# Optimization experiments

Hardware: AMD Instinct MI355X
Metric: run time of the kernel (lower is better)

## Reference

```python
import jax, jax.numpy as jnp
import numpy as np

B, W, I, S, T, U, US = 4, 2000, 64, 64, 24, 32, 2
V, H, D, OUT = 32000, 4, 256, 512
PER = W + I + S + U + 1          # nodes per graph = 2161
N = B * PER                      # 8644 nodes
E_RAND = N * 16


def setup_inputs() -> dict:
    key = jax.random.key(0)
    ks = jax.random.split(key, 24)
    s = 0.02
    inp = {}
    inp["all_words"] = jax.random.randint(ks[0], (B * W,), 0, V)
    inp["image_feats"] = jax.random.normal(ks[1], (B * I, 2048), jnp.float32)
    inp["sentences"] = jax.random.randint(ks[2], (B, S, T), 0, V)
    inp["sentence_mask"] = jnp.ones((B, S, T), jnp.float32)
    inp["utterances"] = jax.random.randint(ks[3], (B, U, US), 0, S)
    inp["utterance_mask"] = jnp.ones((B, U, US), jnp.float32)
    inp["session_ids"] = (jnp.arange(B) + 1) * PER - 1   # last node of each graph
    src = jax.random.randint(ks[4], (E_RAND,), 0, N)
    dst = jax.random.randint(ks[5], (E_RAND,), 0, N)
    loop = jnp.arange(N)
    inp["edge_src"] = jnp.concatenate([src, loop])
    inp["edge_dst"] = jnp.concatenate([dst, loop])
    # learned parameters
    inp["word_embed"] = jax.random.normal(ks[6], (V, 300), jnp.float32) * s
    inp["text_fc_w"] = jax.random.normal(ks[7], (300, 1024), jnp.float32) * s
    inp["text_fc_b"] = jnp.zeros((1024,), jnp.float32)
    inp["image_fc_w"] = jax.random.normal(ks[8], (2048, 1024), jnp.float32) * s
    inp["image_fc_b"] = jnp.zeros((1024,), jnp.float32)
    inp["gat0_fc"] = jax.random.normal(ks[9], (1024, H * D), jnp.float32) * s
    inp["gat0_al"] = jax.random.normal(ks[10], (H, D), jnp.float32) * s
    inp["gat0_ar"] = jax.random.normal(ks[11], (H, D), jnp.float32) * s
    inp["gat0_b"] = jnp.zeros((H * D,), jnp.float32)
    inp["gat1_fc"] = jax.random.normal(ks[12], (H * D, H * D), jnp.float32) * s
    inp["gat1_al"] = jax.random.normal(ks[13], (H, D), jnp.float32) * s
    inp["gat1_ar"] = jax.random.normal(ks[14], (H, D), jnp.float32) * s
    inp["gat1_b"] = jnp.zeros((H * D,), jnp.float32)
    inp["gat2_fc"] = jax.random.normal(ks[15], (H * D, OUT), jnp.float32) * s
    inp["gat2_al"] = jax.random.normal(ks[16], (1, OUT), jnp.float32) * s
    inp["gat2_ar"] = jax.random.normal(ks[17], (1, OUT), jnp.float32) * s
    inp["gat2_b"] = jnp.zeros((OUT,), jnp.float32)
    return inp


def _gat_layer(h, src, dst, fc_w, al, ar, b, act):
    # DGL GATConv: fc -> per-head attention logits -> edge softmax over dst -> aggregate
    n = h.shape[0]
    nh, dd = al.shape
    f = (h @ fc_w).reshape(n, nh, dd)                    # [N,H,D]
    el = (f * al).sum(-1)                                # [N,H]
    er = (f * ar).sum(-1)
    e = jax.nn.leaky_relu(el[src] + er[dst], 0.2)        # [E,H]
    m = jax.ops.segment_max(e, dst, num_segments=n)      # stable softmax per dst node
    a = jnp.exp(e - m[dst])
    z = jax.ops.segment_sum(a, dst, num_segments=n)
    alpha = a / z[dst]                                   # [E,H]
    out = jax.ops.segment_sum(alpha[:, :, None] * f[src], dst, num_segments=n)
    out = out + b.reshape(nh, dd)
    if act:
        out = jax.nn.elu(out)
    return out.reshape(n, nh * dd)


def _masked_mean(x, mask):
    # x: [..., K, F], mask: [..., K]
    s = (x * mask[..., None]).sum(-2)
    cnt = mask.sum(-1, keepdims=True)
    cnt = jnp.where(cnt == 0, 1.0, cnt)
    return s / cnt


def reference(all_words, image_feats, sentences, sentence_mask, utterances,
              utterance_mask, session_ids, edge_src, edge_dst,
              word_embed, text_fc_w, text_fc_b, image_fc_w, image_fc_b,
              gat0_fc, gat0_al, gat0_ar, gat0_b,
              gat1_fc, gat1_al, gat1_ar, gat1_b,
              gat2_fc, gat2_al, gat2_ar, gat2_b):
    b, s_num, t_num = sentences.shape
    u_num, us_num = utterances.shape[1], utterances.shape[2]
    w_per = all_words.shape[0] // b
    i_per = image_feats.shape[0] // b

    # word nodes
    we = word_embed[all_words].reshape(b, w_per, 300)
    # sentence nodes: masked mean over words
    sw = word_embed[sentences]                           # [B,S,T,300]
    sent = _masked_mean(sw, sentence_mask)               # [B,S,300]
    # utterance nodes: gather sentence embeds, masked mean over sentences
    uidx = utterances.reshape(b, u_num * us_num)
    ue = jnp.take_along_axis(sent, uidx[:, :, None], axis=1).reshape(b, u_num, us_num, -1)
    utt = _masked_mean(ue, utterance_mask)               # [B,U,300]
    # session node
    sess = utt.mean(axis=1, keepdims=True)               # [B,1,300]

    txt = lambda x: x @ text_fc_w + text_fc_b
    wf, sf, uf, ssf = txt(we), txt(sent), txt(utt), txt(sess)
    imf = (image_feats @ image_fc_w + image_fc_b).reshape(b, i_per, -1)

    # node layout per graph: [words, images, sentences, utterances, session]
    h = jnp.concatenate([wf, imf, sf, uf, ssf], axis=1).reshape(-1, 1024)

    h = _gat_layer(h, edge_src, edge_dst, gat0_fc, gat0_al, gat0_ar, gat0_b, act=True)
    h = _gat_layer(h, edge_src, edge_dst, gat1_fc, gat1_al, gat1_ar, gat1_b, act=True)
    h = _gat_layer(h, edge_src, edge_dst, gat2_fc, gat2_al, gat2_ar, gat2_b, act=False)

    return h[session_ids]                                # [B, 512]
```

## Files before the change

kernel.cpp:

```cpp
#include <hip/hip_runtime.h>
#include <math.h>

constexpr int kB = 4, kW = 2000, kI = 64, kS = 64, kT = 24, kU = 32, kUS = 2;
constexpr int kPER = kW + kI + kS + kU + 1;
constexpr int kN   = kB * kPER;
constexpr int kTxtPer  = kW + kS + kU + 1;
constexpr int kTxtRows = kB * kTxtPer;
constexpr int kEmb = 300;
constexpr int kEmbPad = 320;
constexpr int kHid = 1024;
constexpr int kOut = 512;
constexpr int kCap = 256;
constexpr int kMaxDeg = 256;
constexpr int kNcB = 1152;
constexpr int kNB  = kN / 4;

typedef __attribute__((ext_vector_type(8))) short bf16x8;
typedef __attribute__((ext_vector_type(4))) float f32x4;
typedef __attribute__((ext_vector_type(2))) float f32x2;

__device__ __forceinline__ unsigned short f2bf(float f) {
  union { float f; unsigned int u; } x; x.f = f;
  unsigned int r = x.u + 0x7FFF + ((x.u >> 16) & 1);
  return (unsigned short)(r >> 16);
}
__device__ __forceinline__ float bf2f(unsigned short u) {
  union { unsigned int u; float f; } x; x.u = ((unsigned int)u) << 16;
  return x.f;
}
__device__ __forceinline__ float bflo(unsigned int u) {
  union { unsigned int u; float f; } x; x.u = u << 16; return x.f;
}
__device__ __forceinline__ float bfhi(unsigned int u) {
  union { unsigned int u; float f; } x; x.u = u & 0xFFFF0000u; return x.f;
}
__device__ __forceinline__ f32x2 bfpair(unsigned int u) {
  union { unsigned int ui[2]; f32x2 f; } x;
  x.ui[0] = u << 16;
  x.ui[1] = u & 0xFFFF0000u;
  return x.f;
}

__device__ __forceinline__ void gl16(const unsigned short* g, unsigned short* l) {
  __builtin_amdgcn_global_load_lds(
      (const __attribute__((address_space(1))) void*)g,
      (__attribute__((address_space(3))) void*)l,
      16, 0, 0);
}

__global__ __launch_bounds__(256) void k_prep0(
    const float* __restrict__ tx_w, unsigned short* __restrict__ o_tx,
    const float* __restrict__ im_w, unsigned short* __restrict__ o_im,
    const float* __restrict__ g0_w, unsigned short* __restrict__ o_g0,
    const float* __restrict__ g1_w, unsigned short* __restrict__ o_g1,
    const float* __restrict__ g2_w, unsigned short* __restrict__ o_g2,
    const float* __restrict__ img, unsigned short* __restrict__ o_img,
    const int* __restrict__ sents, const float* __restrict__ smask,
    const float* __restrict__ wemb, float* __restrict__ sent,
    int* __restrict__ rmt, int* __restrict__ rmi,
    int* __restrict__ cnt, float* __restrict__ Cimg, float* __restrict__ Cg2) {
  int b = blockIdx.x;
  int tid = threadIdx.x;
  int tx = tid & 31, ty = tid >> 5;

  const float* in = nullptr; unsigned short* out = nullptr; int K = 0, N = 0, Kpad = 0, nbx = 0;
  if (b < 320)                { in = tx_w; out = o_tx; K = kEmb; N = kHid; Kpad = kEmbPad; nbx = 32; }
  else if ((b -= 320) < 2048) { in = im_w; out = o_im; K = 2048; N = kHid; Kpad = 2048; nbx = 32; }
  else if ((b -= 2048) < 1024){ in = g0_w; out = o_g0; K = kHid; N = kHid; Kpad = kHid; nbx = 32; }
  else if ((b -= 1024) < 1024){ in = g1_w; out = o_g1; K = kHid; N = kHid; Kpad = kHid; nbx = 32; }
  else if ((b -= 1024) < 512) { in = g2_w; out = o_g2; K = kHid; N = kOut; Kpad = kHid; nbx = 16; }
  else if ((b -= 512) < 512) {
    int i = b * 1024 + tid * 4;
    float4 v = *(const float4*)(img + i);
    ushort4 o; o.x = f2bf(v.x); o.y = f2bf(v.y); o.z = f2bf(v.z); o.w = f2bf(v.w);
    *(ushort4*)(o_img + i) = o;
    return;
  } else if ((b -= 512) < 256) {
    __shared__ int idx[kT];
    __shared__ float mk[kT];
    __shared__ float s_cnt;
    if (tid < kT) { idx[tid] = sents[b * kT + tid]; mk[tid] = smask[b * kT + tid]; }
    __syncthreads();
    if (tid == 0) {
      float c = 0.f;
      for (int i = 0; i < kT; ++i) c += mk[i];
      s_cnt = (c == 0.f) ? 1.f : c;
    }
    __syncthreads();
    for (int d = tid; d < kEmb; d += 256) {
      float acc = 0.f;
      for (int i = 0; i < kT; ++i) acc += wemb[idx[i] * kEmb + d] * mk[i];
      sent[b * kEmb + d] = acc / s_cnt;
    }
    return;
  } else if ((b -= 256) < 34) {
    int i = b * 256 + tid;
    if (i < kTxtRows) {
      int g = i / kTxtPer, j = i - g * kTxtPer;
      int base = g * kPER;
      int node;
      if (j < kW)                 node = base + j;
      else if (j < kW + kS)       node = base + kW + kI + (j - kW);
      else if (j < kW + kS + kU)  node = base + kW + kI + kS + (j - kW - kS);
      else                        node = base + kW + kI + kS + kU;
      rmt[i] = node;
    }
    if (i < kB * kI) {
      int g = i >> 6;
      rmi[i] = g * kPER + kW + (i & 63);
    }
    return;
  } else if ((b -= 34) < 34) {
    int i = b * 256 + tid;
    if (i < kN) cnt[i] = 0;
    return;
  } else if ((b -= 34) < 256) {
    uint4 z = make_uint4(0u, 0u, 0u, 0u);
    ((uint4*)Cimg)[b * 256 + tid] = z;
    return;
  } else if ((b -= 256) < 128) {
    uint4 z = make_uint4(0u, 0u, 0u, 0u);
    ((uint4*)Cg2)[b * 256 + tid] = z;
    return;
  } else {
    b -= 128;
    int i = b * 256 + tid;
    uint4 z = make_uint4(0u, 0u, 0u, 0u);
    ((uint4*)(o_g0 + (size_t)1032 * kHid))[i] = z;
    ((uint4*)(o_g1 + (size_t)1032 * kHid))[i] = z;
    return;
  }

  int bx = b % nbx, by = b / nbx;
  __shared__ float t[32][33];
  int n = bx * 32 + tx;
#pragma unroll
  for (int j = 0; j < 4; ++j) {
    int k = by * 32 + ty + j * 8;
    t[ty + j * 8][tx] = (k < K) ? in[(size_t)k * N + n] : 0.f;
  }
  __syncthreads();
#pragma unroll
  for (int j = 0; j < 4; ++j) {
    int nn = bx * 32 + ty + j * 8;
    int kk = by * 32 + tx;
    out[(size_t)nn * Kpad + kk] = f2bf(t[tx][ty + j * 8]);
  }
}

__global__ __launch_bounds__(256) void k_utt_sess(const int* __restrict__ utts,
                                                  const float* __restrict__ umask,
                                                  const float* __restrict__ sent,
                                                  float* __restrict__ utt,
                                                  float* __restrict__ sess,
                                                  const float* __restrict__ g0_w,
                                                  const float* __restrict__ g1_w,
                                                  const float* __restrict__ g0_al,
                                                  const float* __restrict__ g0_ar,
                                                  const float* __restrict__ g1_al,
                                                  const float* __restrict__ g1_ar,
                                                  unsigned short* __restrict__ o_g0,
                                                  unsigned short* __restrict__ o_g1) {
  int blk = blockIdx.x;
  int tid = threadIdx.x;
  if (blk < kB * kU) {
    int bu = blk, b = bu / kU;
    __shared__ int idx[kUS];
    __shared__ float mk[kUS];
    __shared__ float s_cnt;
    if (tid < kUS) { idx[tid] = utts[bu * kUS + tid]; mk[tid] = umask[bu * kUS + tid]; }
    __syncthreads();
    if (tid == 0) {
      float c = 0.f;
      for (int i = 0; i < kUS; ++i) c += mk[i];
      s_cnt = (c == 0.f) ? 1.f : c;
    }
    __syncthreads();
    for (int d = tid; d < kEmb; d += 256) {
      float acc = 0.f;
      for (int i = 0; i < kUS; ++i) acc += sent[(b * kS + idx[i]) * kEmb + d] * mk[i];
      utt[bu * kEmb + d] = acc / s_cnt;
    }
  } else if (blk < kB * kU + kB) {
    int b = blk - kB * kU;
    for (int d = tid; d < kEmb; d += 256) {
      float acc = 0.f;
      for (int u = 0; u < kU; ++u) {
        float ua = 0.f, c = 0.f;
        for (int us = 0; us < kUS; ++us) {
          int i = (b * kU + u) * kUS + us;
          int sidx = utts[i];
          float m = umask[i];
          ua += sent[(b * kS + sidx) * kEmb + d] * m;
          c += m;
        }
        if (c == 0.f) c = 1.f;
        acc += ua / c;
      }
      sess[b * kEmb + d] = acc * (1.f / kU);
    }
  } else {
    int b = blk - (kB * kU + kB);
    int layer = b >> 7, rem = b & 127;
    int which = rem >> 6;
    int rem2 = rem & 63;
    int h = rem2 >> 4, kblk = rem2 & 15;
    const float* fc = layer ? g1_w : g0_w;
    const float* a  = layer ? (which ? g1_ar : g1_al) : (which ? g0_ar : g0_al);
    unsigned short* wt = layer ? o_g1 : o_g0;
    int kl = tid >> 2, q = tid & 3;
    int k = kblk * 64 + kl;
    float s = 0.f;
    const float* fr = fc + (size_t)k * kHid + h * 256 + q * 64;
    const float* av = a + h * 256 + q * 64;
    for (int d = 0; d < 64; ++d) s += fr[d] * av[d];
    s += __shfl_xor(s, 1);
    s += __shfl_xor(s, 2);
    if (q == 0) wt[(size_t)(1024 + which * 4 + h) * kHid + k] = f2bf(s);
  }
}

__global__ __launch_bounds__(256) void k_txtcount(const int* __restrict__ aw,
                                                  const float* __restrict__ wemb,
                                                  const float* __restrict__ sent,
                                                  const float* __restrict__ utt,
                                                  const float* __restrict__ sess,
                                                  unsigned short* __restrict__ txt,
                                                  const int* __restrict__ dst,
                                                  int* __restrict__ cnt, int E) {
  int blk = blockIdx.x;
  int tid = threadIdx.x;
  if (blk < kTxtRows) {
    int r = blk;
    int g = r / kTxtPer, j = r - g * kTxtPer;
    const float* src;
    if (j < kW)                 src = wemb + (size_t)aw[g * kW + j] * kEmb;
    else if (j < kW + kS)       src = sent + (size_t)(g * kS + (j - kW)) * kEmb;
    else if (j < kW + kS + kU)  src = utt  + (size_t)(g * kU + (j - kW - kS)) * kEmb;
    else                        src = sess + (size_t)g * kEmb;
    for (int d = tid; d < kEmbPad; d += 256)
      txt[(size_t)r * kEmbPad + d] = (d < kEmb) ? f2bf(src[d]) : (unsigned short)0;
  } else {
    int e = (blk - kTxtRows) * 256 + tid;
    if (e < E) atomicAdd(&cnt[dst[e]], 1);
  }
}

template <bool OBF, bool ELR>
__global__ __launch_bounds__(512) void k_mm2(const unsigned short* __restrict__ A,
                                             const unsigned short* __restrict__ Bt,
                                             const float* __restrict__ bias,
                                             const int* __restrict__ rmap,
                                             void* __restrict__ Cout,
                                             float* __restrict__ el,
                                             float* __restrict__ er,
                                             int M, int K, int NcB, int NcOut) {
  __shared__ __align__(16) unsigned short As[128 * 64];
  __shared__ __align__(16) unsigned short Bs[128 * 64];
  int nCol = NcB >> 7;
  int bi = blockIdx.x;
  int xcd = bi & 7, bj = bi >> 3;
  int colTile = bj % nCol;
  int rowTile = ((bj / nCol) << 3) + xcd;
  int row0 = rowTile << 7;
  if (row0 >= M) return;
  int col0 = colTile << 7;

  int tid = threadIdx.x;
  int wid = tid >> 6, lane = tid & 63, quad = lane >> 4, l16 = lane & 15;
  int wm = wid >> 1, wn = wid & 1;

  f32x4 acc[2][4];
  f32x4 zero4 = {0.f, 0.f, 0.f, 0.f};
#pragma unroll
  for (int i = 0; i < 2; ++i)
#pragma unroll
    for (int j = 0; j < 4; ++j) acc[i][j] = zero4;

  int lr = lane >> 3;
  int swc = (lane & 7) ^ lr;

  for (int k0 = 0; k0 < K; k0 += 64) {
    __syncthreads();
#pragma unroll
    for (int i = 0; i < 2; ++i) {
      int rb = i * 64 + wid * 8;
      int r = rb + lr;
      int grow = row0 + r;
      if (grow >= M) grow = row0;
      gl16(A + (size_t)grow * K + k0 + (swc << 3), &As[rb * 64]);
      int nrow = col0 + r;
      gl16(Bt + (size_t)nrow * K + k0 + (swc << 3), &Bs[rb * 64]);
    }
    __syncthreads();
#pragma unroll
    for (int s = 0; s < 2; ++s) {
      int cc = s * 4 + quad;
      bf16x8 aF[2], bF[4];
#pragma unroll
      for (int mi = 0; mi < 2; ++mi) {
        int r = wm * 32 + mi * 16 + l16;
        aF[mi] = *(const bf16x8*)&As[r * 64 + ((cc ^ (r & 7)) << 3)];
      }
#pragma unroll
      for (int ni = 0; ni < 4; ++ni) {
        int r = wn * 64 + ni * 16 + l16;
        bF[ni] = *(const bf16x8*)&Bs[r * 64 + ((cc ^ (r & 7)) << 3)];
      }
#pragma unroll
      for (int mi = 0; mi < 2; ++mi)
#pragma unroll
        for (int ni = 0; ni < 4; ++ni)
          acc[mi][ni] = __builtin_amdgcn_mfma_f32_16x16x32_bf16(aF[mi], bF[ni], acc[mi][ni], 0, 0, 0);
    }
  }

#pragma unroll
  for (int mi = 0; mi < 2; ++mi) {
#pragma unroll
    for (int ni = 0; ni < 4; ++ni) {
      int gm0 = row0 + wm * 32 + mi * 16 + quad * 4;
      int gn  = col0 + wn * 64 + ni * 16 + l16;
      float bv = (bias && gn < NcOut) ? bias[gn] : 0.f;
#pragma unroll
      for (int i = 0; i < 4; ++i) {
        int r = gm0 + i;
        if (r >= M) continue;
        float v = acc[mi][ni][i] + bv;
        if (gn < NcOut) {
          if (OBF) {
            int orow = rmap ? rmap[r] : r;
            ((unsigned short*)Cout)[(size_t)orow * NcOut + gn] = f2bf(v);
          } else {
            ((float*)Cout)[(size_t)r * NcOut + gn] = v;
          }
        } else if (ELR) {
          int gn2 = gn - NcOut;
          if (gn2 < 4)      el[r * 4 + gn2] = v;
          else if (gn2 < 8) er[r * 4 + gn2 - 4] = v;
        }
      }
    }
  }
}

__global__ __launch_bounds__(256) void k_mm_sk(const unsigned short* __restrict__ A,
                                               const unsigned short* __restrict__ Bt,
                                               const int* __restrict__ rowlist,
                                               float* __restrict__ C,
                                               int M, int K, int Nc, int Kc) {
  __shared__ __align__(16) unsigned short As[64 * 64];
  __shared__ __align__(16) unsigned short Bs[64 * 64];
  int tid = threadIdx.x;
  int wid = tid >> 6, lane = tid & 63, quad = lane >> 4, l16 = lane & 15;
  int row0 = blockIdx.y * 64, col0 = blockIdx.x * 64;
  int k0 = blockIdx.z * Kc;
  int k1 = k0 + Kc; if (k1 > K) k1 = K;

  f32x4 acc[4];
  f32x4 zero4 = {0.f, 0.f, 0.f, 0.f};
#pragma unroll
  for (int i = 0; i < 4; ++i) acc[i] = zero4;

  int lr = lane >> 3;
  int swc = (lane & 7) ^ lr;

  int arow[2];
#pragma unroll
  for (int i = 0; i < 2; ++i) {
    int grow = row0 + i * 32 + wid * 8 + lr;
    int ar = 0;
    if (grow < M) ar = rowlist ? rowlist[grow] : grow;
    arow[i] = ar;
  }

  for (int kk = k0; kk < k1; kk += 64) {
    __syncthreads();
#pragma unroll
    for (int i = 0; i < 2; ++i) {
      int rb = i * 32 + wid * 8;
      gl16(A + (size_t)arow[i] * K + kk + (swc << 3), &As[rb * 64]);
      int nrow = col0 + rb + lr;
      gl16(Bt + (size_t)nrow * K + kk + (swc << 3), &Bs[rb * 64]);
    }
    __syncthreads();
#pragma unroll
    for (int s = 0; s < 2; ++s) {
      int cc = s * 4 + quad;
      bf16x8 bF;
      {
        int r = wid * 16 + l16;
        bF = *(const bf16x8*)&Bs[r * 64 + ((cc ^ (r & 7)) << 3)];
      }
#pragma unroll
      for (int mi = 0; mi < 4; ++mi) {
        int r = mi * 16 + l16;
        bf16x8 aF = *(const bf16x8*)&As[r * 64 + ((cc ^ (r & 7)) << 3)];
        acc[mi] = __builtin_amdgcn_mfma_f32_16x16x32_bf16(aF, bF, acc[mi], 0, 0, 0);
      }
    }
  }
#pragma unroll
  for (int mi = 0; mi < 4; ++mi) {
#pragma unroll
    for (int i = 0; i < 4; ++i) {
      int r = row0 + mi * 16 + quad * 4 + i;
      int c = col0 + wid * 16 + l16;
      if (r < M) atomicAdd(&C[(size_t)r * Nc + c], acc[mi][i]);
    }
  }
}

__global__ void k_sk_epi(const float* __restrict__ Cw, const float* __restrict__ bias,
                         const int* __restrict__ rmap, unsigned short* __restrict__ out,
                         int M, int Nc) {
  int i = blockIdx.x * blockDim.x + threadIdx.x;
  if (i >= M * Nc) return;
  int r = i / Nc, c = i - r * Nc;
  out[(size_t)rmap[r] * Nc + c] = f2bf(Cw[i] + bias[c]);
}

__global__ void k_scan(int* __restrict__ deg, int* __restrict__ offs, int n) {
  __shared__ int part[1024];
  int tid = threadIdx.x;
  int per = (n + 1023) >> 10;
  int start = tid * per;
  int local = 0;
  for (int i = 0; i < per; ++i) { int idx = start + i; if (idx < n) local += deg[idx]; }
  part[tid] = local;
  __syncthreads();
  for (int off = 1; off < 1024; off <<= 1) {
    int add = (tid >= off) ? part[tid - off] : 0;
    __syncthreads();
    part[tid] += add;
    __syncthreads();
  }
  int run = (tid == 0) ? 0 : part[tid - 1];
  for (int i = 0; i < per; ++i) {
    int idx = start + i;
    if (idx < n) { offs[idx] = run; run += deg[idx]; }
  }
  if (tid == 1023) offs[n] = part[1023];
  __syncthreads();
  for (int i = tid; i < n; i += 1024) deg[i] = 0;
}

__global__ void k_fill(const int* __restrict__ src, const int* __restrict__ dst,
                       const int* __restrict__ offs, int* __restrict__ cur,
                       int* __restrict__ csr, int E) {
  int e = blockIdx.x * blockDim.x + threadIdx.x;
  if (e < E) {
    int d = dst[e];
    int slot = offs[d] + atomicAdd(&cur[d], 1);
    csr[slot] = src[e];
  }
}

__global__ __launch_bounds__(256) void k_agg3h(const unsigned short* __restrict__ f,
                                               const float* __restrict__ el,
                                               const float* __restrict__ er,
                                               const int* __restrict__ offs,
                                               const int* __restrict__ csr,
                                               const float* __restrict__ bias,
                                               unsigned short* __restrict__ out) {
  __shared__ uint2 ws[4][kMaxDeg];
  int bid = blockIdx.x;
  int xcd = bid & 7;
  int g = xcd & 3;
  int hh = xcd >> 2;
  int nb = bid >> 3;
  if (nb >= kNB) return;
  int tid = threadIdx.x;
  int wid = tid >> 6, lane = tid & 63;
  int v = nb * 4 + wid;

  int e0 = offs[v];
  int deg = offs[v + 1] - e0;
  if (deg > kMaxDeg) deg = kMaxDeg;

  float erv = er[v * 4 + g];

  if (deg <= 64) {
    int s = 0;
    float x = -1e30f;
    if (lane < deg) {
      s = csr[e0 + lane];
      x = el[s * 4 + g] + erv;
      x = x > 0.f ? x : 0.2f * x;
    }
    float m = x;
#pragma unroll
    for (int o = 32; o; o >>= 1) m = fmaxf(m, __shfl_xor(m, o));
    float w = expf(x - m);
    float zs = w;
#pragma unroll
    for (int o = 32; o; o >>= 1) zs += __shfl_xor(zs, o);
    w *= 1.f / zs;
    ws[wid][lane] = make_uint2(__float_as_uint(w), (unsigned)s);
  } else {
    float m = -1e30f;
    for (int base = 0; base < deg; base += 64) {
      int idx = base + lane;
      float x = -1e30f;
      if (idx < deg) {
        int s = csr[e0 + idx];
        x = el[s * 4 + g] + erv;
        x = x > 0.f ? x : 0.2f * x;
        ws[wid][idx] = make_uint2(__float_as_uint(x), (unsigned)s);
      }
      float mm = x;
#pragma unroll
      for (int o = 32; o; o >>= 1) mm = fmaxf(mm, __shfl_xor(mm, o));
      m = fmaxf(m, mm);
    }
    float zs = 0.f;
    for (int base = 0; base < deg; base += 64) {
      int idx = base + lane;
      if (idx < deg) {
        float w = expf(__uint_as_float(ws[wid][idx].x) - m);
        ws[wid][idx].x = __float_as_uint(w);
        zs += w;
      }
    }
#pragma unroll
    for (int o = 32; o; o >>= 1) zs += __shfl_xor(zs, o);
    float rz = 1.f / zs;
    for (int base = 0; base < deg; base += 64) {
      int idx = base + lane;
      if (idx < deg)
        ws[wid][idx].x = __float_as_uint(__uint_as_float(ws[wid][idx].x) * rz);
    }
  }

  int slot = lane >> 4, l16 = lane & 15;
  const char* fb = (const char*)f + (size_t)(g * 256 + hh * 128 + l16 * 8) * 2;
  f32x2 a01 = {0.f, 0.f}, a23 = {0.f, 0.f}, a45 = {0.f, 0.f}, a67 = {0.f, 0.f};
  f32x2 c01 = {0.f, 0.f}, c23 = {0.f, 0.f}, c45 = {0.f, 0.f}, c67 = {0.f, 0.f};
  int e = 0;
  for (; e + 8 <= deg; e += 8) {
    int i0 = e + slot, i1 = e + 4 + slot;
    uint2 t0 = ws[wid][i0]; uint2 t1 = ws[wid][i1];
    uint4 f0 = *(const uint4*)(fb + ((size_t)t0.y << 11));
    uint4 f1 = *(const uint4*)(fb + ((size_t)t1.y << 11));
    float w0 = __uint_as_float(t0.x), w1 = __uint_as_float(t1.x);
    f32x2 wv0 = {w0, w0}, wv1 = {w1, w1};
    a01 += wv0 * bfpair(f0.x); a23 += wv0 * bfpair(f0.y);
    a45 += wv0 * bfpair(f0.z); a67 += wv0 * bfpair(f0.w);
    c01 += wv1 * bfpair(f1.x); c23 += wv1 * bfpair(f1.y);
    c45 += wv1 * bfpair(f1.z); c67 += wv1 * bfpair(f1.w);
  }
  for (; e < deg; e += 4) {
    int idx = e + slot;
    if (idx < deg) {
      uint2 t = ws[wid][idx];
      uint4 fv = *(const uint4*)(fb + ((size_t)t.y << 11));
      float w = __uint_as_float(t.x);
      f32x2 wv = {w, w};
      a01 += wv * bfpair(fv.x); a23 += wv * bfpair(fv.y);
      a45 += wv * bfpair(fv.z); a67 += wv * bfpair(fv.w);
    }
  }
  a01 += c01; a23 += c23; a45 += c45; a67 += c67;
  float a0 = a01.x, a1 = a01.y, a2 = a23.x, a3 = a23.y;
  float a4 = a45.x, a5 = a45.y, a6 = a67.x, a7 = a67.y;
#pragma unroll
  for (int o = 16; o <= 32; o <<= 1) {
    a0 += __shfl_xor(a0, o); a1 += __shfl_xor(a1, o);
    a2 += __shfl_xor(a2, o); a3 += __shfl_xor(a3, o);
    a4 += __shfl_xor(a4, o); a5 += __shfl_xor(a5, o);
    a6 += __shfl_xor(a6, o); a7 += __shfl_xor(a7, o);
  }

  if (slot == 0) {
    int d0 = g * 256 + hh * 128 + l16 * 8;
    float4 b0 = *(const float4*)(bias + d0);
    float4 b1 = *(const float4*)(bias + d0 + 4);
    float o0 = a0 + b0.x, o1 = a1 + b0.y, o2 = a2 + b0.z, o3 = a3 + b0.w;
    float o4 = a4 + b1.x, o5 = a5 + b1.y, o6 = a6 + b1.z, o7 = a7 + b1.w;
    o0 = o0 > 0.f ? o0 : expm1f(o0);
    o1 = o1 > 0.f ? o1 : expm1f(o1);
    o2 = o2 > 0.f ? o2 : expm1f(o2);
    o3 = o3 > 0.f ? o3 : expm1f(o3);
    o4 = o4 > 0.f ? o4 : expm1f(o4);
    o5 = o5 > 0.f ? o5 : expm1f(o5);
    o6 = o6 > 0.f ? o6 : expm1f(o6);
    o7 = o7 > 0.f ? o7 : expm1f(o7);
    uint4 ov;
    ov.x = (unsigned)f2bf(o0) | ((unsigned)f2bf(o1) << 16);
    ov.y = (unsigned)f2bf(o2) | ((unsigned)f2bf(o3) << 16);
    ov.z = (unsigned)f2bf(o4) | ((unsigned)f2bf(o5) << 16);
    ov.w = (unsigned)f2bf(o6) | ((unsigned)f2bf(o7) << 16);
    *(uint4*)(out + (size_t)v * 1024 + d0) = ov;
  }
}

__global__ void k_rows2(const int* __restrict__ sid, const int* __restrict__ offs,
                        const int* __restrict__ csr, int* __restrict__ rowlist,
                        int* __restrict__ info) {
  __shared__ int degs[kB], starts[kB], total;
  int tid = threadIdx.x;
  int bv = tid >> 6, lane = tid & 63;
  if (tid < kB) {
    int v = sid[tid];
    degs[tid] = offs[v + 1] - offs[v];
  }
  __syncthreads();
  if (tid == 0) {
    int p = 0;
    for (int b = 0; b < kB; ++b) {
      starts[b] = p;
      int d = degs[b];
      if (p + d > kCap) d = kCap - p;
      degs[b] = d;
      p += d;
    }
    total = p;
  }
  __syncthreads();
  int v = sid[bv];
  int e0 = offs[v];
  int deg = degs[bv];
  int start = starts[bv];
  if (lane == 0) {
    info[bv] = start;
    info[4 + bv] = deg;
    info[8 + bv] = start;
  }
  __syncthreads();
  for (int idx = lane; idx < deg; idx += 64) {
    int s = csr[e0 + idx];
    rowlist[start + idx] = s;
    if (s == v) info[8 + bv] = start + idx;
  }
  for (int i = total + tid; i < kCap; i += 256) rowlist[i] = 0;
}

__global__ __launch_bounds__(256) void k_gat2fin(const float* __restrict__ fc,
                                                 const float* __restrict__ al,
                                                 const float* __restrict__ ar,
                                                 const int* __restrict__ info,
                                                 const float* __restrict__ bias,
                                                 float* __restrict__ out) {
  __shared__ float el_s[kCap], er_s[kCap];
  int bv = blockIdx.x;
  int tid = threadIdx.x;
  int wid = tid >> 6, lane = tid & 63;
  int start = info[bv], cnt = info[4 + bv];
  int selfI = info[8 + bv] - start;

  for (int i = wid; i < cnt; i += 4) {
    const float* row = fc + (size_t)(start + i) * 512 + lane * 8;
    float4 x0 = *(const float4*)(row);
    float4 x1 = *(const float4*)(row + 4);
    float4 a0 = *(const float4*)(al + lane * 8);
    float4 a1 = *(const float4*)(al + lane * 8 + 4);
    float4 r0 = *(const float4*)(ar + lane * 8);
    float4 r1 = *(const float4*)(ar + lane * 8 + 4);
    float a = x0.x * a0.x + x0.y * a0.y + x0.z * a0.z + x0.w * a0.w
            + x1.x * a1.x + x1.y * a1.y + x1.z * a1.z + x1.w * a1.w;
    float b = x0.x * r0.x + x0.y * r0.y + x0.z * r0.z + x0.w * r0.w
            + x1.x * r1.x + x1.y * r1.y + x1.z * r1.z + x1.w * r1.w;
#pragma unroll
    for (int o = 32; o; o >>= 1) {
      a += __shfl_xor(a, o);
      b += __shfl_xor(b, o);
    }
    if (lane == 0) { el_s[i] = a; er_s[i] = b; }
  }
  __syncthreads();

  float erv = er_s[selfI];
  float m = -1e30f;
  for (int i = 0; i < cnt; ++i) {
    float x = el_s[i] + erv;
    x = x > 0.f ? x : 0.2f * x;
    m = fmaxf(m, x);
  }
  float z = 0.f, s0 = 0.f, s1 = 0.f;
  for (int i = 0; i < cnt; ++i) {
    float x = el_s[i] + erv;
    x = x > 0.f ? x : 0.2f * x;
    float w = expf(x - m);
    z += w;
    s0 += w * fc[(size_t)(start + i) * 512 + tid];
    s1 += w * fc[(size_t)(start + i) * 512 + 256 + tid];
  }
  out[bv * 512 + tid] = s0 / z + bias[tid];
  out[bv * 512 + 256 + tid] = s1 / z + bias[256 + tid];
}

extern "C" void kernel_launch(void* const* d_in, const int* in_sizes, int n_in,
                              void* d_out, int out_size, void* d_ws, size_t ws_size,
                              hipStream_t stream) {
  const int*   all_words   = (const int*)d_in[0];
  const float* image_feats = (const float*)d_in[1];
  const int*   sentences   = (const int*)d_in[2];
  const float* sent_mask   = (const float*)d_in[3];
  const int*   utterances  = (const int*)d_in[4];
  const float* utt_mask    = (const float*)d_in[5];
  const int*   session_ids = (const int*)d_in[6];
  const int*   edge_src    = (const int*)d_in[7];
  const int*   edge_dst    = (const int*)d_in[8];
  const float* word_embed  = (const float*)d_in[9];
  const float* text_fc_w   = (const float*)d_in[10];
  const float* text_fc_b   = (const float*)d_in[11];
  const float* image_fc_w  = (const float*)d_in[12];
  const float* image_fc_b  = (const float*)d_in[13];
  const float* gat0_fc     = (const float*)d_in[14];
  const float* gat0_al     = (const float*)d_in[15];
  const float* gat0_ar     = (const float*)d_in[16];
  const float* gat0_b      = (const float*)d_in[17];
  const float* gat1_fc     = (const float*)d_in[18];
  const float* gat1_al     = (const float*)d_in[19];
  const float* gat1_ar     = (const float*)d_in[20];
  const float* gat1_b      = (const float*)d_in[21];
  const float* gat2_fc     = (const float*)d_in[22];
  const float* gat2_al     = (const float*)d_in[23];
  const float* gat2_ar     = (const float*)d_in[24];
  const float* gat2_b      = (const float*)d_in[25];

  const int E = in_sizes[7];

  char* base = (char*)d_ws;
  size_t off = 0;
  auto alloc = [&](size_t elems, size_t esz) -> void* {
    void* p = base + off;
    off += ((elems * esz + 255) / 256) * 256;
    return p;
  };
  unsigned short* Abf   = (unsigned short*)alloc((size_t)kN * kHid, 2);
  unsigned short* fbf   = (unsigned short*)alloc((size_t)kN * kHid, 2);
  unsigned short* txtbf = (unsigned short*)alloc((size_t)kTxtRows * kEmbPad, 2);
  unsigned short* imgbf = (unsigned short*)alloc((size_t)kB * kI * 2048, 2);
  unsigned short* wtTx  = (unsigned short*)alloc((size_t)kHid * kEmbPad, 2);
  unsigned short* wtIm  = (unsigned short*)alloc((size_t)kHid * 2048, 2);
  unsigned short* wtG0  = (unsigned short*)alloc((size_t)kNcB * kHid, 2);
  unsigned short* wtG1  = (unsigned short*)alloc((size_t)kNcB * kHid, 2);
  unsigned short* wtG2  = (unsigned short*)alloc((size_t)kOut * kHid, 2);
  float* Cimg   = (float*)alloc((size_t)kB * kI * kHid, 4);
  float* Cg2    = (float*)alloc((size_t)kCap * kOut, 4);
  float* sentb  = (float*)alloc((size_t)kB * kS * kEmb, 4);
  float* uttb   = (float*)alloc((size_t)kB * kU * kEmb, 4);
  float* sessb  = (float*)alloc((size_t)kB * kEmb, 4);
  float* el     = (float*)alloc((size_t)kN * 4, 4);
  float* er     = (float*)alloc((size_t)kN * 4, 4);
  int*   offs   = (int*)alloc(kN + 1, 4);
  int*   cnt    = (int*)alloc(kN, 4);
  int*   csr    = (int*)alloc(E, 4);
  int*   rmt    = (int*)alloc(kTxtRows, 4);
  int*   rmi    = (int*)alloc(kB * kI, 4);
  int*   rowl   = (int*)alloc(kCap, 4);
  int*   info   = (int*)alloc(16, 4);
  (void)ws_size; (void)n_in; (void)out_size;

  constexpr int kPrepBlocks = 320 + 2048 + 1024 + 1024 + 512 + 512 + 256 + 34 + 34 + 256 + 128 + 60;
  k_prep0<<<kPrepBlocks, 256, 0, stream>>>(
      text_fc_w, wtTx, image_fc_w, wtIm, gat0_fc, wtG0, gat1_fc, wtG1, gat2_fc, wtG2,
      image_feats, imgbf, sentences, sent_mask, word_embed, sentb, rmt, rmi,
      cnt, Cimg, Cg2);

  k_utt_sess<<<kB * kU + kB + 256, 256, 0, stream>>>(
      utterances, utt_mask, sentb, uttb, sessb,
      gat0_fc, gat1_fc, gat0_al, gat0_ar, gat1_al, gat1_ar, wtG0, wtG1);

  k_txtcount<<<kTxtRows + (E + 255) / 256, 256, 0, stream>>>(
      all_words, word_embed, sentb, uttb, sessb, txtbf, edge_dst, cnt, E);

  k_scan<<<1, 1024, 0, stream>>>(cnt, offs, kN);
  k_fill<<<(E + 255) / 256, 256, 0, stream>>>(edge_src, edge_dst, offs, cnt, csr, E);

  auto mmGrid = [](int M, int NcB_) {
    int nrt = (M + 127) / 128;
    return 8 * (NcB_ / 128) * ((nrt + 7) / 8);
  };

  k_mm2<true, false><<<mmGrid(kTxtRows, kHid), 512, 0, stream>>>(
      txtbf, wtTx, text_fc_b, rmt, Abf, nullptr, nullptr, kTxtRows, kEmbPad, kHid, kHid);

  k_mm_sk<<<dim3(kHid / 64, kB * kI / 64, 4), 256, 0, stream>>>(
      imgbf, wtIm, nullptr, Cimg, kB * kI, 2048, kHid, 512);
  k_sk_epi<<<(kB * kI * kHid + 255) / 256, 256, 0, stream>>>(
      Cimg, image_fc_b, rmi, Abf, kB * kI, kHid);

  k_mm2<true, true><<<mmGrid(kN, kNcB), 512, 0, stream>>>(
      Abf, wtG0, nullptr, nullptr, fbf, el, er, kN, kHid, kNcB, kHid);
  k_agg3h<<<8 * kNB, 256, 0, stream>>>(fbf, el, er, offs, csr, gat0_b, Abf);

  k_mm2<true, true><<<mmGrid(kN, kNcB), 512, 0, stream>>>(
      Abf, wtG1, nullptr, nullptr, fbf, el, er, kN, kHid, kNcB, kHid);
  k_agg3h<<<8 * kNB, 256, 0, stream>>>(fbf, el, er, offs, csr, gat1_b, Abf);

  k_rows2<<<1, 256, 0, stream>>>(session_ids, offs, csr, rowl, info);
  k_mm_sk<<<dim3(kOut / 64, kCap / 64, 4), 256, 0, stream>>>(
      Abf, wtG2, rowl, Cg2, kCap, kHid, kOut, 256);
  k_gat2fin<<<kB, 256, 0, stream>>>(Cg2, gat2_al, gat2_ar, info, gat2_b, (float*)d_out);
}
```

Before: 409.1 us.

## Split GAT aggregation into edge-softmax weight kernel and per-head gather kernel

Replaces the fused softmax-plus-aggregation kernel with two kernels. The first computes the edge softmax weights for all four heads at once and writes them to a global per-head weight array. The second gathers neighbour features, with each lane covering four channels of a full 256-wide head, and streams indices and weights straight from global memory. This removes the per-block redundant softmax work across the 8 head/half blocks and the LDS staging, at the cost of an extra launch and a global weight buffer round trip. It also drops the degree cap of 256.

```diff
diff --git a/kernel.cpp b/kernel.cpp
--- a/kernel.cpp
+++ b/kernel.cpp
@@ -11,9 +11,9 @@
 constexpr int kHid = 1024;
 constexpr int kOut = 512;
 constexpr int kCap = 256;
-constexpr int kMaxDeg = 256;
 constexpr int kNcB = 1152;
 constexpr int kNB  = kN / 4;
+constexpr int kNBhi = (kNB + 1) / 2;
 
 typedef __attribute__((ext_vector_type(8))) short bf16x8;
 typedef __attribute__((ext_vector_type(4))) float f32x4;
@@ -27,12 +27,6 @@
 __device__ __forceinline__ float bf2f(unsigned short u) {
   union { unsigned int u; float f; } x; x.u = ((unsigned int)u) << 16;
   return x.f;
-}
-__device__ __forceinline__ float bflo(unsigned int u) {
-  union { unsigned int u; float f; } x; x.u = u << 16; return x.f;
-}
-__device__ __forceinline__ float bfhi(unsigned int u) {
-  union { unsigned int u; float f; } x; x.u = u & 0xFFFF0000u; return x.f;
 }
 __device__ __forceinline__ f32x2 bfpair(unsigned int u) {
   union { unsigned int ui[2]; f32x2 f; } x;
@@ -456,142 +450,173 @@
   }
 }
 
-__global__ __launch_bounds__(256) void k_agg3h(const unsigned short* __restrict__ f,
-                                               const float* __restrict__ el,
+__global__ __launch_bounds__(256) void k_smaxw(const float* __restrict__ el,
                                                const float* __restrict__ er,
                                                const int* __restrict__ offs,
                                                const int* __restrict__ csr,
-                                               const float* __restrict__ bias,
-                                               unsigned short* __restrict__ out) {
-  __shared__ uint2 ws[4][kMaxDeg];
-  int bid = blockIdx.x;
-  int xcd = bid & 7;
-  int g = xcd & 3;
-  int hh = xcd >> 2;
-  int nb = bid >> 3;
-  if (nb >= kNB) return;
+                                               float* __restrict__ wcsr, int E) {
   int tid = threadIdx.x;
   int wid = tid >> 6, lane = tid & 63;
-  int v = nb * 4 + wid;
-
+  int v = blockIdx.x * 4 + wid;
   int e0 = offs[v];
   int deg = offs[v + 1] - e0;
-  if (deg > kMaxDeg) deg = kMaxDeg;
-
-  float erv = er[v * 4 + g];
+  float4 erv = *(const float4*)(er + (size_t)v * 4);
 
   if (deg <= 64) {
-    int s = 0;
-    float x = -1e30f;
+    float x0 = -1e30f, x1 = -1e30f, x2 = -1e30f, x3 = -1e30f;
     if (lane < deg) {
-      s = csr[e0 + lane];
-      x = el[s * 4 + g] + erv;
-      x = x > 0.f ? x : 0.2f * x;
-    }
-    float m = x;
-#pragma unroll
-    for (int o = 32; o; o >>= 1) m = fmaxf(m, __shfl_xor(m, o));
-    float w = expf(x - m);
-    float zs = w;
-#pragma unroll
-    for (int o = 32; o; o >>= 1) zs += __shfl_xor(zs, o);
-    w *= 1.f / zs;
-    ws[wid][lane] = make_uint2(__float_as_uint(w), (unsigned)s);
+      int s = csr[e0 + lane];
+      float4 e4 = *(const float4*)(el + (size_t)s * 4);
+      x0 = e4.x + erv.x; x1 = e4.y + erv.y; x2 = e4.z + erv.z; x3 = e4.w + erv.w;
+      x0 = x0 > 0.f ? x0 : 0.2f * x0;
+      x1 = x1 > 0.f ? x1 : 0.2f * x1;
+      x2 = x2 > 0.f ? x2 : 0.2f * x2;
+      x3 = x3 > 0.f ? x3 : 0.2f * x3;
+    }
+    float m0 = x0, m1 = x1, m2 = x2, m3 = x3;
+#pragma unroll
+    for (int o = 32; o; o >>= 1) {
+      m0 = fmaxf(m0, __shfl_xor(m0, o));
+      m1 = fmaxf(m1, __shfl_xor(m1, o));
+      m2 = fmaxf(m2, __shfl_xor(m2, o));
+      m3 = fmaxf(m3, __shfl_xor(m3, o));
+    }
+    float w0 = expf(x0 - m0), w1 = expf(x1 - m1);
+    float w2 = expf(x2 - m2), w3 = expf(x3 - m3);
+    float z0 = w0, z1 = w1, z2 = w2, z3 = w3;
+#pragma unroll
+    for (int o = 32; o; o >>= 1) {
+      z0 += __shfl_xor(z0, o); z1 += __shfl_xor(z1, o);
+      z2 += __shfl_xor(z2, o); z3 += __shfl_xor(z3, o);
+    }
+    if (lane < deg) {
+      wcsr[(size_t)0 * E + e0 + lane] = w0 / z0;
+      wcsr[(size_t)1 * E + e0 + lane] = w1 / z1;
+      wcsr[(size_t)2 * E + e0 + lane] = w2 / z2;
+      wcsr[(size_t)3 * E + e0 + lane] = w3 / z3;
+    }
   } else {
-    float m = -1e30f;
-    for (int base = 0; base < deg; base += 64) {
-      int idx = base + lane;
-      float x = -1e30f;
-      if (idx < deg) {
-        int s = csr[e0 + idx];
-        x = el[s * 4 + g] + erv;
-        x = x > 0.f ? x : 0.2f * x;
-        ws[wid][idx] = make_uint2(__float_as_uint(x), (unsigned)s);
-      }
-      float mm = x;
-#pragma unroll
-      for (int o = 32; o; o >>= 1) mm = fmaxf(mm, __shfl_xor(mm, o));
-      m = fmaxf(m, mm);
-    }
-    float zs = 0.f;
+    float m0 = -1e30f, m1 = -1e30f, m2 = -1e30f, m3 = -1e30f;
     for (int base = 0; base < deg; base += 64) {
       int idx = base + lane;
       if (idx < deg) {
-        float w = expf(__uint_as_float(ws[wid][idx].x) - m);
-        ws[wid][idx].x = __float_as_uint(w);
-        zs += w;
+        int s = csr[e0 + idx];
+        float4 e4 = *(const float4*)(el + (size_t)s * 4);
+        float x0 = e4.x + erv.x, x1 = e4.y + erv.y, x2 = e4.z + erv.z, x3 = e4.w + erv.w;
+        x0 = x0 > 0.f ? x0 : 0.2f * x0;
+        x1 = x1 > 0.f ? x1 : 0.2f * x1;
+        x2 = x2 > 0.f ? x2 : 0.2f * x2;
+        x3 = x3 > 0.f ? x3 : 0.2f * x3;
+        m0 = fmaxf(m0, x0); m1 = fmaxf(m1, x1);
+        m2 = fmaxf(m2, x2); m3 = fmaxf(m3, x3);
       }
     }
 #pragma unroll
-    for (int o = 32; o; o >>= 1) zs += __shfl_xor(zs, o);
-    float rz = 1.f / zs;
+    for (int o = 32; o; o >>= 1) {
+      m0 = fmaxf(m0, __shfl_xor(m0, o));
+      m1 = fmaxf(m1, __shfl_xor(m1, o));
+      m2 = fmaxf(m2, __shfl_xor(m2, o));
+      m3 = fmaxf(m3, __shfl_xor(m3, o));
+    }
+    float z0 = 0.f, z1 = 0.f, z2 = 0.f, z3 = 0.f;
     for (int base = 0; base < deg; base += 64) {
       int idx = base + lane;
-      if (idx < deg)
-        ws[wid][idx].x = __float_as_uint(__uint_as_float(ws[wid][idx].x) * rz);
-    }
-  }
-
-  int slot = lane >> 4, l16 = lane & 15;
-  const char* fb = (const char*)f + (size_t)(g * 256 + hh * 128 + l16 * 8) * 2;
-  f32x2 a01 = {0.f, 0.f}, a23 = {0.f, 0.f}, a45 = {0.f, 0.f}, a67 = {0.f, 0.f};
-  f32x2 c01 = {0.f, 0.f}, c23 = {0.f, 0.f}, c45 = {0.f, 0.f}, c67 = {0.f, 0.f};
+      if (idx < deg) {
+        int s = csr[e0 + idx];
+        float4 e4 = *(const float4*)(el + (size_t)s * 4);
+        float x0 = e4.x + erv.x, x1 = e4.y + erv.y, x2 = e4.z + erv.z, x3 = e4.w + erv.w;
+        x0 = x0 > 0.f ? x0 : 0.2f * x0;
+        x1 = x1 > 0.f ? x1 : 0.2f * x1;
+        x2 = x2 > 0.f ? x2 : 0.2f * x2;
+        x3 = x3 > 0.f ? x3 : 0.2f * x3;
+        float w0 = expf(x0 - m0), w1 = expf(x1 - m1);
+        float w2 = expf(x2 - m2), w3 = expf(x3 - m3);
+        wcsr[(size_t)0 * E + e0 + idx] = w0;
+        wcsr[(size_t)1 * E + e0 + idx] = w1;
+        wcsr[(size_t)2 * E + e0 + idx] = w2;
+        wcsr[(size_t)3 * E + e0 + idx] = w3;
+        z0 += w0; z1 += w1; z2 += w2; z3 += w3;
+      }
+    }
+#pragma unroll
+    for (int o = 32; o; o >>= 1) {
+      z0 += __shfl_xor(z0, o); z1 += __shfl_xor(z1, o);
+      z2 += __shfl_xor(z2, o); z3 += __shfl_xor(z3, o);
+    }
+    float r0 = 1.f / z0, r1 = 1.f / z1, r2 = 1.f / z2, r3 = 1.f / z3;
+    for (int base = 0; base < deg; base += 64) {
+      int idx = base + lane;
+      if (idx < deg) {
+        wcsr[(size_t)0 * E + e0 + idx] *= r0;
+        wcsr[(size_t)1 * E + e0 + idx] *= r1;
+        wcsr[(size_t)2 * E + e0 + idx] *= r2;
+        wcsr[(size_t)3 * E + e0 + idx] *= r3;
+      }
+    }
+  }
+}
+
+__global__ __launch_bounds__(256) void k_aggs(const unsigned short* __restrict__ f,
+                                              const int* __restrict__ offs,
+                                              const int* __restrict__ csr,
+                                              const float* __restrict__ wcsr,
+                                              const float* __restrict__ bias,
+                                              unsigned short* __restrict__ out, int E) {
+  int bid = blockIdx.x;
+  int xcd = bid & 7;
+  int h = xcd & 3;
+  int nb = (xcd >> 2) * kNBhi + (bid >> 3);
+  if (nb >= kNB) return;
+  int tid = threadIdx.x;
+  int wid = tid >> 6, lane = tid & 63;
+  int v = nb * 4 + wid;
+
+  int e0 = __builtin_amdgcn_readfirstlane(offs[v]);
+  int deg = __builtin_amdgcn_readfirstlane(offs[v + 1]) - e0;
+
+  const int* cs = csr + e0;
+  const float* wp = wcsr + (size_t)h * E + e0;
+  const unsigned short* fb = f + h * 256 + lane * 4;
+
+  f32x2 a0 = {0.f, 0.f}, a1 = {0.f, 0.f};
+  f32x2 b0 = {0.f, 0.f}, b1 = {0.f, 0.f};
+  f32x2 c0 = {0.f, 0.f}, c1 = {0.f, 0.f};
+  f32x2 d0 = {0.f, 0.f}, d1 = {0.f, 0.f};
   int e = 0;
-  for (; e + 8 <= deg; e += 8) {
-    int i0 = e + slot, i1 = e + 4 + slot;
-    uint2 t0 = ws[wid][i0]; uint2 t1 = ws[wid][i1];
-    uint4 f0 = *(const uint4*)(fb + ((size_t)t0.y << 11));
-    uint4 f1 = *(const uint4*)(fb + ((size_t)t1.y << 11));
-    float w0 = __uint_as_float(t0.x), w1 = __uint_as_float(t1.x);
-    f32x2 wv0 = {w0, w0}, wv1 = {w1, w1};
-    a01 += wv0 * bfpair(f0.x); a23 += wv0 * bfpair(f0.y);
-    a45 += wv0 * bfpair(f0.z); a67 += wv0 * bfpair(f0.w);
-    c01 += wv1 * bfpair(f1.x); c23 += wv1 * bfpair(f1.y);
-    c45 += wv1 * bfpair(f1.z); c67 += wv1 * bfpair(f1.w);
-  }
-  for (; e < deg; e += 4) {
-    int idx = e + slot;
-    if (idx < deg) {
-      uint2 t = ws[wid][idx];
-      uint4 fv = *(const uint4*)(fb + ((size_t)t.y << 11));
-      float w = __uint_as_float(t.x);
-      f32x2 wv = {w, w};
-      a01 += wv * bfpair(fv.x); a23 += wv * bfpair(fv.y);
-      a45 += wv * bfpair(fv.z); a67 += wv * bfpair(fv.w);
-    }
-  }
-  a01 += c01; a23 += c23; a45 += c45; a67 += c67;
-  float a0 = a01.x, a1 = a01.y, a2 = a23.x, a3 = a23.y;
-  float a4 = a45.x, a5 = a45.y, a6 = a67.x, a7 = a67.y;
-#pragma unroll
-  for (int o = 16; o <= 32; o <<= 1) {
-    a0 += __shfl_xor(a0, o); a1 += __shfl_xor(a1, o);
-    a2 += __shfl_xor(a2, o); a3 += __shfl_xor(a3, o);
-    a4 += __shfl_xor(a4, o); a5 += __shfl_xor(a5, o);
-    a6 += __shfl_xor(a6, o); a7 += __shfl_xor(a7, o);
-  }
-
-  if (slot == 0) {
-    int d0 = g * 256 + hh * 128 + l16 * 8;
-    float4 b0 = *(const float4*)(bias + d0);
-    float4 b1 = *(const float4*)(bias + d0 + 4);
-    float o0 = a0 + b0.x, o1 = a1 + b0.y, o2 = a2 + b0.z, o3 = a3 + b0.w;
-    float o4 = a4 + b1.x, o5 = a5 + b1.y, o6 = a6 + b1.z, o7 = a7 + b1.w;
-    o0 = o0 > 0.f ? o0 : expm1f(o0);
-    o1 = o1 > 0.f ? o1 : expm1f(o1);
-    o2 = o2 > 0.f ? o2 : expm1f(o2);
-    o3 = o3 > 0.f ? o3 : expm1f(o3);
-    o4 = o4 > 0.f ? o4 : expm1f(o4);
-    o5 = o5 > 0.f ? o5 : expm1f(o5);
-    o6 = o6 > 0.f ? o6 : expm1f(o6);
-    o7 = o7 > 0.f ? o7 : expm1f(o7);
-    uint4 ov;
-    ov.x = (unsigned)f2bf(o0) | ((unsigned)f2bf(o1) << 16);
-    ov.y = (unsigned)f2bf(o2) | ((unsigned)f2bf(o3) << 16);
-    ov.z = (unsigned)f2bf(o4) | ((unsigned)f2bf(o5) << 16);
-    ov.w = (unsigned)f2bf(o6) | ((unsigned)f2bf(o7) << 16);
-    *(uint4*)(out + (size_t)v * 1024 + d0) = ov;
-  }
+  for (; e + 4 <= deg; e += 4) {
+    int s0 = cs[e], s1 = cs[e + 1], s2 = cs[e + 2], s3 = cs[e + 3];
+    float w0 = wp[e], w1 = wp[e + 1], w2 = wp[e + 2], w3 = wp[e + 3];
+    uint2 q0 = *(const uint2*)(fb + ((size_t)s0 << 10));
+    uint2 q1 = *(const uint2*)(fb + ((size_t)s1 << 10));
+    uint2 q2 = *(const uint2*)(fb + ((size_t)s2 << 10));
+    uint2 q3 = *(const uint2*)(fb + ((size_t)s3 << 10));
+    f32x2 wv0 = {w0, w0}, wv1 = {w1, w1}, wv2 = {w2, w2}, wv3 = {w3, w3};
+    a0 += wv0 * bfpair(q0.x); a1 += wv0 * bfpair(q0.y);
+    b0 += wv1 * bfpair(q1.x); b1 += wv1 * bfpair(q1.y);
+    c0 += wv2 * bfpair(q2.x); c1 += wv2 * bfpair(q2.y);
+    d0 += wv3 * bfpair(q3.x); d1 += wv3 * bfpair(q3.y);
+  }
+  for (; e < deg; ++e) {
+    int s0 = cs[e];
+    float w0 = wp[e];
+    uint2 q0 = *(const uint2*)(fb + ((size_t)s0 << 10));
+    f32x2 wv0 = {w0, w0};
+    a0 += wv0 * bfpair(q0.x); a1 += wv0 * bfpair(q0.y);
+  }
+  a0 += b0; c0 += d0; a0 += c0;
+  a1 += b1; c1 += d1; a1 += c1;
+
+  int dd = h * 256 + lane * 4;
+  float4 bv = *(const float4*)(bias + dd);
+  float o0 = a0.x + bv.x, o1 = a0.y + bv.y, o2 = a1.x + bv.z, o3 = a1.y + bv.w;
+  o0 = o0 > 0.f ? o0 : expm1f(o0);
+  o1 = o1 > 0.f ? o1 : expm1f(o1);
+  o2 = o2 > 0.f ? o2 : expm1f(o2);
+  o3 = o3 > 0.f ? o3 : expm1f(o3);
+  uint2 ov;
+  ov.x = (unsigned)f2bf(o0) | ((unsigned)f2bf(o1) << 16);
+  ov.y = (unsigned)f2bf(o2) | ((unsigned)f2bf(o3) << 16);
+  *(uint2*)(out + (size_t)v * 1024 + dd) = ov;
 }
 
 __global__ void k_rows2(const int* __restrict__ sid, const int* __restrict__ offs,
@@ -744,6 +769,7 @@
   float* sessb  = (float*)alloc((size_t)kB * kEmb, 4);
   float* el     = (float*)alloc((size_t)kN * 4, 4);
   float* er     = (float*)alloc((size_t)kN * 4, 4);
+  float* wcsr   = (float*)alloc((size_t)E * 4, 4);
   int*   offs   = (int*)alloc(kN + 1, 4);
   int*   cnt    = (int*)alloc(kN, 4);
   int*   csr    = (int*)alloc(E, 4);
@@ -784,11 +810,13 @@
 
   k_mm2<true, true><<<mmGrid(kN, kNcB), 512, 0, stream>>>(
       Abf, wtG0, nullptr, nullptr, fbf, el, er, kN, kHid, kNcB, kHid);
-  k_agg3h<<<8 * kNB, 256, 0, stream>>>(fbf, el, er, offs, csr, gat0_b, Abf);
+  k_smaxw<<<kNB, 256, 0, stream>>>(el, er, offs, csr, wcsr, E);
+  k_aggs<<<8 * kNBhi, 256, 0, stream>>>(fbf, offs, csr, wcsr, gat0_b, Abf, E);
 
   k_mm2<true, true><<<mmGrid(kN, kNcB), 512, 0, stream>>>(
       Abf, wtG1, nullptr, nullptr, fbf, el, er, kN, kHid, kNcB, kHid);
-  k_agg3h<<<8 * kNB, 256, 0, stream>>>(fbf, el, er, offs, csr, gat1_b, Abf);
+  k_smaxw<<<kNB, 256, 0, stream>>>(el, er, offs, csr, wcsr, E);
+  k_aggs<<<8 * kNBhi, 256, 0, stream>>>(fbf, offs, csr, wcsr, gat1_b, Abf, E);
 
   k_rows2<<<1, 256, 0, stream>>>(session_ids, offs, csr, rowl, info);
   k_mm_sk<<<dim3(kOut / 64, kCap / 64, 4), 256, 0, stream>>>(
```

Result: faster. 383.9 us (-6.2%).
